# Kernel tuning notes

Hardware: AMD Instinct MI355X
Metric: run time of the kernel (lower is better)

## Reference

```python
import jax, jax.numpy as jnp
import numpy as np

B, L, H, E, D = 4, 2048, 8, 64, 64  # seq S == L (causal mask requires square scores)


def setup_inputs() -> dict:
    key = jax.random.key(0)
    k0, k1, k2, k3, k4 = jax.random.split(key, 5)
    queries = jax.random.normal(k0, (B, L, H, E), jnp.float32)
    keys = jax.random.normal(k1, (B, L, H, E), jnp.float32)
    values = jax.random.normal(k2, (B, L, H, D), jnp.float32)
    # per-sample learned de-stationary scale (positive) and bias
    tau = jax.random.uniform(k3, (B, 1, 1), jnp.float32, 0.5, 1.5)
    delta = jax.random.normal(k4, (B, 1, L), jnp.float32) * 0.1
    return {"queries": queries, "keys": keys, "values": values, "tau": tau, "delta": delta}


def reference(queries, keys, values, tau, delta):
    Bq, Lq, Hq, Eq = queries.shape
    S = keys.shape[1]
    scale = 1.0 / jnp.sqrt(jnp.asarray(Eq, jnp.float32))
    # torch path: rearrange('b s h d l -> (b d) s h l') with s=h=d=1 -> [B,1,1,1] / [B,1,1,S]
    tau_b = tau.reshape(Bq, 1, 1, 1)
    delta_b = delta.reshape(Bq, 1, 1, -1)[..., :S]
    # scores: [B, H, L, S]
    scores = jnp.einsum('blhe,bshe->bhls', queries, keys) * tau_b + delta_b
    causal = jnp.triu(jnp.ones((Lq, S), bool), k=1)  # True above diagonal -> masked
    scores = jnp.where(causal, -jnp.inf, scores)
    A = jax.nn.softmax(scale * scores, axis=-1)  # dropout is identity in eval/reference
    V = jnp.einsum('bhls,bshd->blhd', A, values)  # [B, L, H, D]
    return V
```

## Files before the change

### kernel.cpp

```cpp
#include <hip/hip_runtime.h>
#include <hip/hip_bf16.h>

#define Bsz 4
#define Lsz 2048
#define Hsz 8

typedef __attribute__((ext_vector_type(8))) short bf16x8;
typedef __attribute__((ext_vector_type(4))) short bf16x4;
typedef __attribute__((ext_vector_type(4))) float f32x4;

__device__ __forceinline__ short f2bs(float f) {
    union { float f; unsigned u; } v; v.f = f;
    unsigned r = v.u + 0x7FFFu + ((v.u >> 16) & 1u);
    return (short)(r >> 16);
}
__device__ __forceinline__ short f2bs_rh(float f) {
    return (short)((__float_as_uint(f) + 0x8000u) >> 16);
}

__device__ __forceinline__ void stage16(const short* g, short* l) {
    __builtin_amdgcn_global_load_lds(
        (const __attribute__((address_space(1))) unsigned int*)g,
        (__attribute__((address_space(3))) unsigned int*)l,
        16, 0, 0);
}

__global__ __launch_bounds__(256) void prep_kv(
    const float* __restrict__ ksrc, const float* __restrict__ vsrc,
    short* __restrict__ Kf, short* __restrict__ Vf)
{
    __shared__ float Tl[64][65];
    const int raw = blockIdx.x;
    const int tid = threadIdx.x;
    const bool isK = raw < Bsz*Hsz*32;
    const int bid = isK ? raw : raw - Bsz*Hsz*32;
    const int tl = bid & 31, bh = bid >> 5;
    const int b = bh >> 3, h = bh & 7;

    const int row = tid >> 2, c0 = (tid & 3) * 16;
    const float* src = (isK ? ksrc : vsrc)
                     + (((size_t)b*Lsz + tl*64 + row)*Hsz + h)*64 + c0;
    *(float4*)&Tl[row][c0]      = *(const float4*)(src);
    *(float4*)&Tl[row][c0 + 4]  = *(const float4*)(src + 4);
    *(float4*)&Tl[row][c0 + 8]  = *(const float4*)(src + 8);
    *(float4*)&Tl[row][c0 + 12] = *(const float4*)(src + 12);
    __syncthreads();

    const int lane = tid & 63, ln = lane & 15, quad = lane >> 4;
    if (isK) {
        short* dst = Kf + (size_t)bid * 4096;
        #pragma unroll
        for (int cc = 0; cc < 2; ++cc) {
            const int c  = (tid >> 6)*2 + cc;
            const int nt = c >> 1, eh = c & 1;
            const float* rp = &Tl[nt*16 + ln][eh*32 + quad*8];
            bf16x8 o = {f2bs(rp[0]),f2bs(rp[1]),f2bs(rp[2]),f2bs(rp[3]),
                        f2bs(rp[4]),f2bs(rp[5]),f2bs(rp[6]),f2bs(rp[7])};
            *(bf16x8*)(dst + c*512 + lane*8) = o;
        }
    } else {
        short* dst = Vf + (size_t)bid * 4096;
        #pragma unroll
        for (int cc = 0; cc < 2; ++cc) {
            const int cp  = (tid >> 6)*2 + cc;
            const int m16 = cp >> 1, nt0 = (cp & 1)*2;
            const int d   = m16*16 + ln;
            const int s0  = nt0*16 + quad*4;
            bf16x8 o = {f2bs(Tl[s0+0][d]),  f2bs(Tl[s0+1][d]),
                        f2bs(Tl[s0+2][d]),  f2bs(Tl[s0+3][d]),
                        f2bs(Tl[s0+16][d]), f2bs(Tl[s0+17][d]),
                        f2bs(Tl[s0+18][d]), f2bs(Tl[s0+19][d])};
            *(bf16x8*)(dst + cp*512 + lane*8) = o;
        }
    }
}

__global__ __launch_bounds__(256, 4) void dsattn_main(
    const float* __restrict__ q,
    const short* __restrict__ Kf,
    const short* __restrict__ Vf,
    const float* __restrict__ tau,
    const float* __restrict__ delta,
    float* __restrict__ out)
{
    __shared__ __align__(16) short Kb[2][4096];
    __shared__ __align__(16) short Vb[2][4096];
    __shared__ float dls[Lsz];

    const int tid  = threadIdx.x;
    const int wv   = tid >> 6;
    const int lane = tid & 63;
    const int ln   = lane & 15;
    const int quad = lane >> 4;

    const int bh = blockIdx.x;
    const int b  = bh >> 3, h = bh & 7;
    const int j  = blockIdx.y, aj = j & 7, gj = j >> 3;
    const int qt = (gj == 0) ? aj : (gj == 1) ? 15 - aj
                 : (gj == 2) ? 16 + aj : 31 - aj;
    const int q0 = qt * 64;
    const int T  = qt + 1;

    const float c2  = 0.125f * 1.44269504f;
    const float st2 = c2 * tau[b];

    const short* kt = Kf + (size_t)bh * (32*4096);
    const short* vt = Vf + (size_t)bh * (32*4096);

    {
        const float* dsrc = delta + (size_t)b*Lsz + tid*8;
        float4 a = *(const float4*)(dsrc);
        float4 c = *(const float4*)(dsrc + 4);
        a.x*=c2; a.y*=c2; a.z*=c2; a.w*=c2;
        c.x*=c2; c.y*=c2; c.z*=c2; c.w*=c2;
        *(float4*)&dls[tid*8]     = a;
        *(float4*)&dls[tid*8 + 4] = c;
    }

    #pragma unroll
    for (int u = 0; u < 4; ++u) {
        const int c = wv*4 + u;
        const short* g = ((c < 8) ? kt : vt) + (c & 7)*512 + lane*8;
        short* l = ((c < 8) ? &Kb[0][0] : &Vb[0][0]) + (c & 7)*512;
        stage16(g, l);
    }

    bf16x8 qf0, qf1;
    {
        const float* qrow = q + (((size_t)b*Lsz + q0 + wv*16 + ln)*Hsz + h)*64;
        float4 a0 = *(const float4*)(qrow + quad*8);
        float4 a1 = *(const float4*)(qrow + quad*8 + 4);
        float4 b0 = *(const float4*)(qrow + 32 + quad*8);
        float4 b1 = *(const float4*)(qrow + 32 + quad*8 + 4);
        qf0 = (bf16x8){f2bs(a0.x),f2bs(a0.y),f2bs(a0.z),f2bs(a0.w),
                       f2bs(a1.x),f2bs(a1.y),f2bs(a1.z),f2bs(a1.w)};
        qf1 = (bf16x8){f2bs(b0.x),f2bs(b0.y),f2bs(b0.z),f2bs(b0.w),
                       f2bs(b1.x),f2bs(b1.y),f2bs(b1.z),f2bs(b1.w)};
    }

    f32x4 oacc[4];
    #pragma unroll
    for (int m = 0; m < 4; ++m) oacc[m] = (f32x4){0.f,0.f,0.f,0.f};
    float l_acc = 0.f;

    __syncthreads();

    for (int t = 0; t < T; ++t) {
        const int cur = t & 1;
        if (t + 1 < T) {
            const int nb = cur ^ 1;
            #pragma unroll
            for (int u = 0; u < 4; ++u) {
                const int c = wv*4 + u;
                const short* g = ((c < 8) ? kt : vt)
                               + (size_t)(t+1)*4096 + (c & 7)*512 + lane*8;
                short* l = ((c < 8) ? &Kb[nb][0] : &Vb[nb][0]) + (c & 7)*512;
                stage16(g, l);
            }
        }

        const short* Kc = &Kb[cur][0];
        const short* Vc = &Vb[cur][0];
        const int k0 = t*64;

        f32x4 sacc[4];
        #pragma unroll
        for (int nt = 0; nt < 4; ++nt) {
            bf16x8 kf0 = *(const bf16x8*)(Kc + (nt*2+0)*512 + lane*8);
            bf16x8 kf1 = *(const bf16x8*)(Kc + (nt*2+1)*512 + lane*8);
            f32x4 z = (f32x4){0.f,0.f,0.f,0.f};
            z = __builtin_amdgcn_mfma_f32_16x16x32_bf16(kf0, qf0, z, 0,0,0);
            sacc[nt] = __builtin_amdgcn_mfma_f32_16x16x32_bf16(kf1, qf1, z, 0,0,0);
        }

        f32x4 dlv[4];
        #pragma unroll
        for (int nt = 0; nt < 4; ++nt)
            dlv[nt] = *(const f32x4*)&dls[k0 + nt*16 + quad*4];

        if (t == qt) {
            const int qrow = q0 + wv*16 + ln;
            #pragma unroll
            for (int nt = 0; nt < 4; ++nt)
                #pragma unroll
                for (int r = 0; r < 4; ++r)
                    if (k0 + nt*16 + quad*4 + r > qrow) sacc[nt][r] = -1e30f;
        }
        bf16x4 pT[4];
        #pragma unroll
        for (int nt = 0; nt < 4; ++nt) {
            float p0 = __builtin_amdgcn_exp2f(fmaf(sacc[nt][0], st2, dlv[nt][0]));
            float p1 = __builtin_amdgcn_exp2f(fmaf(sacc[nt][1], st2, dlv[nt][1]));
            float p2 = __builtin_amdgcn_exp2f(fmaf(sacc[nt][2], st2, dlv[nt][2]));
            float p3 = __builtin_amdgcn_exp2f(fmaf(sacc[nt][3], st2, dlv[nt][3]));
            l_acc += (p0 + p1) + (p2 + p3);
            pT[nt] = (bf16x4){f2bs_rh(p0), f2bs_rh(p1), f2bs_rh(p2), f2bs_rh(p3)};
        }

        #pragma unroll
        for (int ntp = 0; ntp < 2; ++ntp)
            #pragma unroll
            for (int m16 = 0; m16 < 4; ++m16) {
                bf16x8 vv = *(const bf16x8*)(Vc + (m16*2+ntp)*512 + lane*8);
                bf16x4 v0 = (bf16x4){vv[0], vv[1], vv[2], vv[3]};
                bf16x4 v1 = (bf16x4){vv[4], vv[5], vv[6], vv[7]};
                oacc[m16] = __builtin_amdgcn_mfma_f32_16x16x16bf16_1k(
                    v0, pT[2*ntp+0], oacc[m16], 0,0,0);
                oacc[m16] = __builtin_amdgcn_mfma_f32_16x16x16bf16_1k(
                    v1, pT[2*ntp+1], oacc[m16], 0,0,0);
            }

        __syncthreads();
    }

    float lsum = l_acc;
    lsum += __shfl_xor(lsum, 16, 64);
    lsum += __shfl_xor(lsum, 32, 64);
    const float inv = 1.0f / lsum;
    const int qrow = q0 + wv*16 + ln;
    float* orow = out + (((size_t)b*Lsz + qrow)*Hsz + h)*64;
    #pragma unroll
    for (int m16 = 0; m16 < 4; ++m16) {
        float4 o = {oacc[m16][0]*inv, oacc[m16][1]*inv,
                    oacc[m16][2]*inv, oacc[m16][3]*inv};
        *(float4*)(orow + m16*16 + quad*4) = o;
    }
}

extern "C" void kernel_launch(void* const* d_in, const int* in_sizes, int n_in,
                              void* d_out, int out_size, void* d_ws, size_t ws_size,
                              hipStream_t stream) {
    (void)in_sizes; (void)n_in; (void)out_size; (void)ws_size;
    const float* q     = (const float*)d_in[0];
    const float* k     = (const float*)d_in[1];
    const float* v     = (const float*)d_in[2];
    const float* tau   = (const float*)d_in[3];
    const float* delta = (const float*)d_in[4];
    float* out = (float*)d_out;

    short* Kf = (short*)d_ws;
    short* Vf = (short*)d_ws + (size_t)(4*1024*1024);

    prep_kv<<<dim3(Bsz*Hsz*32*2), dim3(256), 0, stream>>>(k, v, Kf, Vf);
    dsattn_main<<<dim3(Bsz*Hsz, 32), dim3(256), 0, stream>>>(q, Kf, Vf, tau, delta, out);
}
```

Measured before the change: 128.6 us.

## Split waves into 2x2 query/key grid with LDS partial-output reduction

Restructures the four waves from one 16-row query strip each into a 2x2 grid: each wave handles 32 query rows against half of the 64-key tile, reusing K/V fragments across two query sub-tiles. On the diagonal tile, one wave whose keys are all masked skips its work entirely. Partial outputs and row sums from the two key-half waves are combined through shared memory at the end. This halves per-wave K/V LDS reads per MFMA but doubles accumulator registers and adds an extra reduction/barrier.

```diff
diff --git a/kernel.cpp b/kernel.cpp
--- a/kernel.cpp
+++ b/kernel.cpp
@@ -83,15 +83,18 @@
     const float* __restrict__ delta,
     float* __restrict__ out)
 {
-    __shared__ __align__(16) short Kb[2][4096];
-    __shared__ __align__(16) short Vb[2][4096];
-    __shared__ float dls[Lsz];
+    __shared__ __align__(16) char smem[40960];
+    short* KbBase = (short*)smem;
+    short* VbBase = (short*)(smem + 16384);
+    float* dls    = (float*)(smem + 32768);
 
     const int tid  = threadIdx.x;
     const int wv   = tid >> 6;
     const int lane = tid & 63;
     const int ln   = lane & 15;
     const int quad = lane >> 4;
+    const int qh   = wv >> 1;
+    const int kh   = wv & 1;
 
     const int bh = blockIdx.x;
     const int b  = bh >> 3, h = bh & 7;
@@ -121,27 +124,31 @@
     for (int u = 0; u < 4; ++u) {
         const int c = wv*4 + u;
         const short* g = ((c < 8) ? kt : vt) + (c & 7)*512 + lane*8;
-        short* l = ((c < 8) ? &Kb[0][0] : &Vb[0][0]) + (c & 7)*512;
+        short* l = ((c < 8) ? KbBase : VbBase) + (c & 7)*512;
         stage16(g, l);
     }
 
-    bf16x8 qf0, qf1;
-    {
-        const float* qrow = q + (((size_t)b*Lsz + q0 + wv*16 + ln)*Hsz + h)*64;
+    const int qbase = q0 + qh*32;
+    bf16x8 qf[2][2];
+    #pragma unroll
+    for (int qm = 0; qm < 2; ++qm) {
+        const float* qrow = q + (((size_t)b*Lsz + qbase + qm*16 + ln)*Hsz + h)*64;
         float4 a0 = *(const float4*)(qrow + quad*8);
         float4 a1 = *(const float4*)(qrow + quad*8 + 4);
         float4 b0 = *(const float4*)(qrow + 32 + quad*8);
         float4 b1 = *(const float4*)(qrow + 32 + quad*8 + 4);
-        qf0 = (bf16x8){f2bs(a0.x),f2bs(a0.y),f2bs(a0.z),f2bs(a0.w),
-                       f2bs(a1.x),f2bs(a1.y),f2bs(a1.z),f2bs(a1.w)};
-        qf1 = (bf16x8){f2bs(b0.x),f2bs(b0.y),f2bs(b0.z),f2bs(b0.w),
-                       f2bs(b1.x),f2bs(b1.y),f2bs(b1.z),f2bs(b1.w)};
-    }
-
-    f32x4 oacc[4];
-    #pragma unroll
-    for (int m = 0; m < 4; ++m) oacc[m] = (f32x4){0.f,0.f,0.f,0.f};
-    float l_acc = 0.f;
+        qf[qm][0] = (bf16x8){f2bs(a0.x),f2bs(a0.y),f2bs(a0.z),f2bs(a0.w),
+                             f2bs(a1.x),f2bs(a1.y),f2bs(a1.z),f2bs(a1.w)};
+        qf[qm][1] = (bf16x8){f2bs(b0.x),f2bs(b0.y),f2bs(b0.z),f2bs(b0.w),
+                             f2bs(b1.x),f2bs(b1.y),f2bs(b1.z),f2bs(b1.w)};
+    }
+
+    f32x4 oacc[4][2];
+    #pragma unroll
+    for (int m = 0; m < 4; ++m)
+        #pragma unroll
+        for (int qm = 0; qm < 2; ++qm) oacc[m][qm] = (f32x4){0.f,0.f,0.f,0.f};
+    float l_acc[2] = {0.f, 0.f};
 
     __syncthreads();
 
@@ -154,77 +161,123 @@
                 const int c = wv*4 + u;
                 const short* g = ((c < 8) ? kt : vt)
                                + (size_t)(t+1)*4096 + (c & 7)*512 + lane*8;
-                short* l = ((c < 8) ? &Kb[nb][0] : &Vb[nb][0]) + (c & 7)*512;
+                short* l = ((c < 8) ? KbBase : VbBase) + nb*4096 + (c & 7)*512;
                 stage16(g, l);
             }
         }
 
-        const short* Kc = &Kb[cur][0];
-        const short* Vc = &Vb[cur][0];
-        const int k0 = t*64;
-
-        f32x4 sacc[4];
-        #pragma unroll
-        for (int nt = 0; nt < 4; ++nt) {
-            bf16x8 kf0 = *(const bf16x8*)(Kc + (nt*2+0)*512 + lane*8);
-            bf16x8 kf1 = *(const bf16x8*)(Kc + (nt*2+1)*512 + lane*8);
-            f32x4 z = (f32x4){0.f,0.f,0.f,0.f};
-            z = __builtin_amdgcn_mfma_f32_16x16x32_bf16(kf0, qf0, z, 0,0,0);
-            sacc[nt] = __builtin_amdgcn_mfma_f32_16x16x32_bf16(kf1, qf1, z, 0,0,0);
-        }
-
-        f32x4 dlv[4];
-        #pragma unroll
-        for (int nt = 0; nt < 4; ++nt)
-            dlv[nt] = *(const f32x4*)&dls[k0 + nt*16 + quad*4];
-
-        if (t == qt) {
-            const int qrow = q0 + wv*16 + ln;
-            #pragma unroll
-            for (int nt = 0; nt < 4; ++nt)
-                #pragma unroll
-                for (int r = 0; r < 4; ++r)
-                    if (k0 + nt*16 + quad*4 + r > qrow) sacc[nt][r] = -1e30f;
-        }
-        bf16x4 pT[4];
-        #pragma unroll
-        for (int nt = 0; nt < 4; ++nt) {
-            float p0 = __builtin_amdgcn_exp2f(fmaf(sacc[nt][0], st2, dlv[nt][0]));
-            float p1 = __builtin_amdgcn_exp2f(fmaf(sacc[nt][1], st2, dlv[nt][1]));
-            float p2 = __builtin_amdgcn_exp2f(fmaf(sacc[nt][2], st2, dlv[nt][2]));
-            float p3 = __builtin_amdgcn_exp2f(fmaf(sacc[nt][3], st2, dlv[nt][3]));
-            l_acc += (p0 + p1) + (p2 + p3);
-            pT[nt] = (bf16x4){f2bs_rh(p0), f2bs_rh(p1), f2bs_rh(p2), f2bs_rh(p3)};
-        }
-
-        #pragma unroll
-        for (int ntp = 0; ntp < 2; ++ntp)
+        if (!(t == qt && qh == 0 && kh == 1)) {
+            const short* Kc = KbBase + cur*4096;
+            const short* Vc = VbBase + cur*4096;
+            const int k0 = t*64;
+
+            bf16x8 kfr[2][2];
+            #pragma unroll
+            for (int nl = 0; nl < 2; ++nl)
+                #pragma unroll
+                for (int eh = 0; eh < 2; ++eh)
+                    kfr[nl][eh] = *(const bf16x8*)(Kc + ((2*kh+nl)*2+eh)*512 + lane*8);
+
+            f32x4 sacc[2][2];
+            #pragma unroll
+            for (int qm = 0; qm < 2; ++qm)
+                #pragma unroll
+                for (int nl = 0; nl < 2; ++nl) {
+                    f32x4 z = (f32x4){0.f,0.f,0.f,0.f};
+                    z = __builtin_amdgcn_mfma_f32_16x16x32_bf16(kfr[nl][0], qf[qm][0], z, 0,0,0);
+                    sacc[qm][nl] = __builtin_amdgcn_mfma_f32_16x16x32_bf16(kfr[nl][1], qf[qm][1], z, 0,0,0);
+                }
+
+            f32x4 dlv[2];
+            #pragma unroll
+            for (int nl = 0; nl < 2; ++nl)
+                dlv[nl] = *(const f32x4*)&dls[k0 + kh*32 + nl*16 + quad*4];
+
+            if (t == qt) {
+                #pragma unroll
+                for (int qm = 0; qm < 2; ++qm) {
+                    const int qrow = qbase + qm*16 + ln;
+                    #pragma unroll
+                    for (int nl = 0; nl < 2; ++nl)
+                        #pragma unroll
+                        for (int r = 0; r < 4; ++r)
+                            if (k0 + kh*32 + nl*16 + quad*4 + r > qrow)
+                                sacc[qm][nl][r] = -1e30f;
+                }
+            }
+
+            bf16x4 pT[2][2];
+            #pragma unroll
+            for (int qm = 0; qm < 2; ++qm)
+                #pragma unroll
+                for (int nl = 0; nl < 2; ++nl) {
+                    float p0 = __builtin_amdgcn_exp2f(fmaf(sacc[qm][nl][0], st2, dlv[nl][0]));
+                    float p1 = __builtin_amdgcn_exp2f(fmaf(sacc[qm][nl][1], st2, dlv[nl][1]));
+                    float p2 = __builtin_amdgcn_exp2f(fmaf(sacc[qm][nl][2], st2, dlv[nl][2]));
+                    float p3 = __builtin_amdgcn_exp2f(fmaf(sacc[qm][nl][3], st2, dlv[nl][3]));
+                    l_acc[qm] += (p0 + p1) + (p2 + p3);
+                    pT[qm][nl] = (bf16x4){f2bs_rh(p0), f2bs_rh(p1), f2bs_rh(p2), f2bs_rh(p3)};
+                }
+
             #pragma unroll
             for (int m16 = 0; m16 < 4; ++m16) {
-                bf16x8 vv = *(const bf16x8*)(Vc + (m16*2+ntp)*512 + lane*8);
+                bf16x8 vv = *(const bf16x8*)(Vc + (m16*2+kh)*512 + lane*8);
                 bf16x4 v0 = (bf16x4){vv[0], vv[1], vv[2], vv[3]};
                 bf16x4 v1 = (bf16x4){vv[4], vv[5], vv[6], vv[7]};
-                oacc[m16] = __builtin_amdgcn_mfma_f32_16x16x16bf16_1k(
-                    v0, pT[2*ntp+0], oacc[m16], 0,0,0);
-                oacc[m16] = __builtin_amdgcn_mfma_f32_16x16x16bf16_1k(
-                    v1, pT[2*ntp+1], oacc[m16], 0,0,0);
+                #pragma unroll
+                for (int qm = 0; qm < 2; ++qm) {
+                    oacc[m16][qm] = __builtin_amdgcn_mfma_f32_16x16x16bf16_1k(
+                        v0, pT[qm][0], oacc[m16][qm], 0,0,0);
+                    oacc[m16][qm] = __builtin_amdgcn_mfma_f32_16x16x16bf16_1k(
+                        v1, pT[qm][1], oacc[m16][qm], 0,0,0);
+                }
             }
+        }
 
         __syncthreads();
     }
 
-    float lsum = l_acc;
-    lsum += __shfl_xor(lsum, 16, 64);
-    lsum += __shfl_xor(lsum, 32, 64);
-    const float inv = 1.0f / lsum;
-    const int qrow = q0 + wv*16 + ln;
-    float* orow = out + (((size_t)b*Lsz + qrow)*Hsz + h)*64;
-    #pragma unroll
-    for (int m16 = 0; m16 < 4; ++m16) {
-        float4 o = {oacc[m16][0]*inv, oacc[m16][1]*inv,
-                    oacc[m16][2]*inv, oacc[m16][3]*inv};
-        *(float4*)(orow + m16*16 + quad*4) = o;
-    }
+    float* osc = (float*)smem;
+    float* lx  = (float*)(smem + 20480);
+
+    float lt[2];
+    #pragma unroll
+    for (int qm = 0; qm < 2; ++qm) {
+        float ls = l_acc[qm];
+        ls += __shfl_xor(ls, 16, 64);
+        ls += __shfl_xor(ls, 32, 64);
+        lt[qm] = ls;
+        if (quad == 0) lx[(wv*2+qm)*16 + ln] = ls;
+    }
+    const int wr0 = (1 - kh) * 2;
+    #pragma unroll
+    for (int mm = 0; mm < 2; ++mm)
+        #pragma unroll
+        for (int qm = 0; qm < 2; ++qm) {
+            f32x4 o = oacc[wr0+mm][qm];
+            *(float4*)&osc[(wv*32 + qm*16 + ln)*36 + mm*16 + quad*4] =
+                (float4){o[0], o[1], o[2], o[3]};
+        }
+    __syncthreads();
+
+    const int pw = wv ^ 1;
+    const int st0 = kh * 2;
+    float inv[2];
+    #pragma unroll
+    for (int qm = 0; qm < 2; ++qm)
+        inv[qm] = 1.0f / (lt[qm] + lx[(pw*2+qm)*16 + ln]);
+    #pragma unroll
+    for (int mm = 0; mm < 2; ++mm)
+        #pragma unroll
+        for (int qm = 0; qm < 2; ++qm) {
+            const int m16 = st0 + mm;
+            float4 add = *(const float4*)&osc[(pw*32 + qm*16 + ln)*36 + mm*16 + quad*4];
+            f32x4 o = oacc[m16][qm];
+            float4 res = {(o[0]+add.x)*inv[qm], (o[1]+add.y)*inv[qm],
+                          (o[2]+add.z)*inv[qm], (o[3]+add.w)*inv[qm]};
+            const int qrow = qbase + qm*16 + ln;
+            *(float4*)(out + (((size_t)b*Lsz + qrow)*Hsz + h)*64 + m16*16 + quad*4) = res;
+        }
 }
 
 extern "C" void kernel_launch(void* const* d_in, const int* in_sizes, int n_in,
```

Result: slower. 139.5 us (+8.5%).
